# Optimization experiments

Measured on AMD Instinct MI355X. Metric: run time of the kernel, lower is better.

The kernel has to match this reference:

```python
import jax, jax.numpy as jnp
import numpy as np
import math

HEAD_DIM = 256
NUM_HEADS = 8
NUM_KV_HEADS = 1
ROPE_THETA = 10000.0


def _rope_cos_sin(position_ids, dim, base, dtype):
    # inv_freq: [dim//2]
    inv_freq = 1.0 / (base ** (jnp.arange(0, dim, 2, dtype=jnp.float32) / dim))
    # freqs: [B, S, dim//2]
    freqs = position_ids.astype(jnp.float32)[..., None] * inv_freq[None, None, :]
    emb = jnp.concatenate([freqs, freqs], axis=-1)  # [B, S, dim]
    return jnp.cos(emb).astype(dtype), jnp.sin(emb).astype(dtype)


def _rotate_half(x):
    half = x.shape[-1] // 2
    return jnp.concatenate([-x[..., half:], x[..., :half]], axis=-1)


def setup_inputs() -> dict:
    key = jax.random.key(0)
    ks = jax.random.split(key, 6)
    B, S, H = 2, 2048, 2048
    hidden_states = jax.random.normal(ks[0], (B, S, H), dtype=jnp.float32)
    attention_mask = jnp.zeros((B, 1, S, S), dtype=jnp.float32)
    position_ids = jnp.arange(B * S, dtype=jnp.int64).reshape(B, S) % S
    wq = jax.random.normal(ks[1], (H, NUM_HEADS * HEAD_DIM), dtype=jnp.float32) * 0.02
    wk = jax.random.normal(ks[2], (H, NUM_KV_HEADS * HEAD_DIM), dtype=jnp.float32) * 0.02
    wv = jax.random.normal(ks[3], (H, NUM_KV_HEADS * HEAD_DIM), dtype=jnp.float32) * 0.02
    wo = jax.random.normal(ks[4], (NUM_HEADS * HEAD_DIM, H), dtype=jnp.float32) * 0.02
    return {"hidden_states": hidden_states, "attention_mask": attention_mask,
            "position_ids": position_ids, "wq": wq, "wk": wk, "wv": wv, "wo": wo}


def reference(hidden_states, attention_mask, position_ids, wq, wk, wv, wo):
    B, S, _ = hidden_states.shape
    q = (hidden_states @ wq).reshape(B, S, NUM_HEADS, HEAD_DIM).transpose(0, 2, 1, 3)
    k = (hidden_states @ wk).reshape(B, S, NUM_KV_HEADS, HEAD_DIM).transpose(0, 2, 1, 3)
    v = (hidden_states @ wv).reshape(B, S, NUM_KV_HEADS, HEAD_DIM).transpose(0, 2, 1, 3)

    cos, sin = _rope_cos_sin(position_ids, HEAD_DIM, ROPE_THETA, hidden_states.dtype)
    cos = cos[:, None, :, :]  # [B,1,S,D]
    sin = sin[:, None, :, :]
    q = q * cos + _rotate_half(q) * sin
    k = k * cos + _rotate_half(k) * sin

    # repeat_kv (GQA/MQA expansion)
    n_rep = NUM_HEADS // NUM_KV_HEADS
    k = jnp.repeat(k, n_rep, axis=1)  # [B,H,S,D]
    v = jnp.repeat(v, n_rep, axis=1)

    scores = jnp.einsum('bhqd,bhkd->bhqk', q, k) / math.sqrt(HEAD_DIM)
    scores = scores + attention_mask
    probs = jax.nn.softmax(scores.astype(jnp.float32), axis=-1).astype(q.dtype)
    attn = jnp.einsum('bhqk,bhkd->bhqd', probs, v)  # [B,H,S,D]
    attn = attn.transpose(0, 2, 1, 3).reshape(B, S, NUM_HEADS * HEAD_DIM)
    return attn @ wo
```

## Files before the change

kernel.cpp:

```cpp
#include <hip/hip_runtime.h>
#include <hip/hip_bf16.h>

typedef unsigned short u16;
using f32x4  = __attribute__((ext_vector_type(4))) float;
using bf16x8 = __attribute__((ext_vector_type(8))) __bf16;
using u16x8  = __attribute__((ext_vector_type(8))) unsigned short;
using u16x4  = __attribute__((ext_vector_type(4))) unsigned short;

__device__ __forceinline__ float bf2f(u16 v) {
  union { unsigned u; float f; } x; x.u = ((unsigned)v) << 16; return x.f;
}
__device__ __forceinline__ u16 f2bf(float f) {
  union { float f; unsigned u; } x; x.f = f;
  unsigned r = x.u + 0x7fffu + ((x.u >> 16) & 1u);
  return (u16)(r >> 16);
}
__device__ __forceinline__ void async_load16(const u16* g, u16* l) {
  __builtin_amdgcn_global_load_lds(
      (const __attribute__((address_space(1))) unsigned int*)g,
      (__attribute__((address_space(3))) unsigned int*)l, 16, 0, 0);
}
__device__ __forceinline__ float fexp2(float x) {
#if __has_builtin(__builtin_amdgcn_exp2f)
  return __builtin_amdgcn_exp2f(x);
#else
  return exp2f(x);
#endif
}
__device__ __forceinline__ float vmax4(f32x4 v) {
  return fmaxf(fmaxf(v[0], v[1]), fmaxf(v[2], v[3]));
}
__device__ __forceinline__ int swz_col(int col, int rowk) {
  return (col & ~63) | ((((col >> 3) & 7) ^ rowk) << 3) | (col & 7);
}

__global__ __launch_bounds__(256) void cast_f32_bf16_sw(const float* __restrict__ in,
                                                        u16* __restrict__ out) {
  long i = ((long)blockIdx.x * 256 + threadIdx.x) * 8;
  int m = (int)(i >> 11);
  int col = (int)(i & 2047);
  float4 a = *(const float4*)(in + i);
  float4 b = *(const float4*)(in + i + 4);
  u16x8 v;
  v[0] = f2bf(a.x); v[1] = f2bf(a.y); v[2] = f2bf(a.z); v[3] = f2bf(a.w);
  v[4] = f2bf(b.x); v[5] = f2bf(b.y); v[6] = f2bf(b.z); v[7] = f2bf(b.w);
  *(u16x8*)(out + ((long)m << 11) + swz_col(col, m & 7)) = v;
}

__global__ __launch_bounds__(256) void trans_all(const float* __restrict__ wq,
                                                 const float* __restrict__ wk,
                                                 const float* __restrict__ wv,
                                                 const float* __restrict__ wo,
                                                 u16* __restrict__ wqkvT, u16* __restrict__ woT) {
  const int z = blockIdx.z, bx = blockIdx.x, by = blockIdx.y;
  if (z == 1 && bx >= 64) return;
  const float* src; int srs; u16* dst;
  const int R0 = bx * 32;
  if (z == 0) {
    if (R0 < 2048)      { src = wq + R0;          srs = 2048; }
    else if (R0 < 2304) { src = wk + (R0 - 2048); srs = 256;  }
    else                { src = wv + (R0 - 2304); srs = 256;  }
    dst = wqkvT;
  } else { src = wo + R0; srs = 2048; dst = woT; }
  __shared__ float t[32][33];
  int tx = threadIdx.x, ty = threadIdx.y;
  int br = by * 32;
#pragma unroll
  for (int i = 0; i < 32; i += 8)
    t[ty + i][tx] = src[(long)(br + ty + i) * srs + tx];
  __syncthreads();
#pragma unroll
  for (int i = 0; i < 32; i += 8) {
    int R = R0 + ty + i, C = br + tx;
    dst[(long)R * 2048 + swz_col(C, R & 7)] = f2bf(t[tx][ty + i]);
  }
}

template <typename CT>
__global__ __launch_bounds__(256) void gemm_bt(const u16* __restrict__ A, const u16* __restrict__ Bt,
                                               CT* __restrict__ C, int M, int N, int K) {
  __shared__ __attribute__((aligned(16))) u16 sA[128 * 64];
  __shared__ __attribute__((aligned(16))) u16 sB[128 * 64];
  const int n0 = blockIdx.x * 128, m0 = blockIdx.y * 128;
  const int tid = threadIdx.x;
  const int w = tid >> 6, lane = tid & 63;
  const int l15 = lane & 15, quad = lane >> 4;
  const int wm = (w >> 1) * 64, wn = (w & 1) * 64;
  const int lrow = lane >> 3, lcol = (lane & 7) * 8;
  const u16* Ag = A + (long)(m0 + lrow) * K + lcol;
  const u16* Bg = Bt + (long)(n0 + lrow) * K + lcol;
  const int g0 = ((quad ^ (l15 & 7)) << 3);
  f32x4 acc[4][4] = {};
  for (int k0 = 0; k0 < K; k0 += 64) {
#pragma unroll
    for (int i = 0; i < 4; ++i) {
      int rr = (w * 4 + i) * 8;
      async_load16(Ag + (long)rr * K + k0, &sA[rr * 64]);
      async_load16(Bg + (long)rr * K + k0, &sB[rr * 64]);
    }
    __syncthreads();
#pragma unroll
    for (int kk2 = 0; kk2 < 2; ++kk2) {
      const int go = kk2 ? (g0 ^ 32) : g0;
      bf16x8 af[4], bf[4];
#pragma unroll
      for (int t = 0; t < 4; ++t) {
        af[t] = *(const bf16x8*)&sA[(wm + t * 16 + l15) * 64 + go];
        bf[t] = *(const bf16x8*)&sB[(wn + t * 16 + l15) * 64 + go];
      }
#pragma unroll
      for (int mt = 0; mt < 4; ++mt)
#pragma unroll
        for (int nt = 0; nt < 4; ++nt)
          acc[mt][nt] = __builtin_amdgcn_mfma_f32_16x16x32_bf16(af[mt], bf[nt], acc[mt][nt], 0, 0, 0);
    }
    __syncthreads();
  }
#pragma unroll
  for (int mt = 0; mt < 4; ++mt)
#pragma unroll
    for (int nt = 0; nt < 4; ++nt)
#pragma unroll
      for (int r = 0; r < 4; ++r) {
        long idx = (long)(m0 + wm + mt * 16 + quad * 4 + r) * N + (n0 + wn + nt * 16 + l15);
        if constexpr (sizeof(CT) == 4) C[idx] = acc[mt][nt][r];
        else                           C[idx] = f2bf(acc[mt][nt][r]);
      }
}

__global__ __launch_bounds__(256) void rope_pack(u16* __restrict__ qkv, u16* __restrict__ kp) {
  const int row = blockIdx.x;
  const int tid = threadIdx.x;
  const int d = tid & 127;
  const int s = row & 2047;
  float ang = (float)s * fexp2(-(float)d * 0.10381025296523007f);
  float sn, cs;
  sincosf(ang, &sn, &cs);
  long base = (long)row * 2560;
#pragma unroll
  for (int j = 0; j < 4; ++j) {
    int h = (tid >> 7) + j * 2;
    long p = base + h * 256 + d;
    float x0 = bf2f(qkv[p]), x1 = bf2f(qkv[p + 128]);
    qkv[p]       = f2bf(x0 * cs - x1 * sn);
    qkv[p + 128] = f2bf(x1 * cs + x0 * sn);
  }
  if (tid < 128) {
    long p = base + 2048 + d;
    float x0 = bf2f(qkv[p]), x1 = bf2f(qkv[p + 128]);
    float y0 = x0 * cs - x1 * sn, y1 = x1 * cs + x0 * sn;
    int b = row >> 11, t = (row >> 6) & 31, r = row & 63;
    long sw = (r >> 1) & 7;
    long tb = (long)(b * 32 + t) * 8 * 2048;
#pragma unroll
    for (int u = 0; u < 2; ++u) {
      int D = d + u * 128;
      long off = tb + (long)(D >> 5) * 2048 + r * 32 + (D & 31);
      long off2 = (((off >> 3) ^ sw) << 3) | (off & 7);
      kp[off2] = f2bf(u ? y1 : y0);
    }
  }
}

__global__ __launch_bounds__(256) void pack_vt(const u16* __restrict__ qkv, u16* __restrict__ vp) {
  __shared__ u16 sm[32][40];
  int x = blockIdx.x, y = blockIdx.y, b = blockIdx.z;
  int tx = threadIdx.x, ty = threadIdx.y;
  long inrow = (long)b * 2048 + (y >> 1) * 64 + (y & 1) * 32;
#pragma unroll
  for (int i = 0; i < 32; i += 8)
    sm[ty + i][tx] = qkv[(inrow + ty + i) * 2560 + 2304 + x * 32 + tx];
  __syncthreads();
  long obase = ((long)(b * 32 + (y >> 1)) * 2 + (y & 1)) * 8192 + (long)x * 1024;
#pragma unroll
  for (int i = 0; i < 32; i += 8) {
    long el = obase + (ty + i) * 32 + tx;
    el ^= (long)((((ty + i) >> 1) & 7) << 3);
    vp[el] = sm[tx][ty + i];
  }
}

__global__ __launch_bounds__(512) void flash_attn(const u16* __restrict__ qkv,
                                                  const u16* __restrict__ kp,
                                                  const u16* __restrict__ vp,
                                                  u16* __restrict__ attn) {
  const int qt = blockIdx.x, h = blockIdx.y, b = blockIdx.z;
  const int tid = threadIdx.x, w = tid >> 6, lane = tid & 63;
  const int l15 = lane & 15, quad = lane >> 4;
  __shared__ __attribute__((aligned(16))) u16 sK[2][16384];
  __shared__ __attribute__((aligned(16))) u16 sV[2][16384];
  __shared__ __attribute__((aligned(16))) u16 sP[8][1152];
  const long rowb = (long)b * 2048;
  const int qrow0 = qt * 128 + w * 16;
  const int swz_rd = (l15 >> 1) * 64 + ((((l15 & 1) << 2) | quad) ^ (l15 >> 1)) * 8;

  bf16x8 aq[8];
  {
    const u16* qp = qkv + (rowb + qrow0 + l15) * 2560 + h * 256 + quad * 8;
#pragma unroll
    for (int kk = 0; kk < 8; ++kk) aq[kk] = *(const bf16x8*)(qp + kk * 32);
  }

  float m_i = -1e30f, l_i = 0.f;
  f32x4 accO[16] = {};
  const float SC = 0.09016844005556021f;

  u16* Pw = &sP[w][0];
  const u16* kpb = kp + (long)b * 32 * 16384;
  const u16* vpb = vp + (long)b * 32 * 16384;

#pragma unroll
  for (int j = 0; j < 4; ++j) {
    int base = (w * 4 + j) * 512;
    async_load16(kpb + base + lane * 8, &sK[0][base]);
    async_load16(vpb + base + lane * 8, &sV[0][base]);
  }
  __syncthreads();

  for (int it = 0; it < 32; ++it) {
    const int cur = it & 1;
    const int nx = (it < 31) ? it + 1 : 31;
    const u16* ktn = kpb + (long)nx * 16384;
    const u16* vtn = vpb + (long)nx * 16384;
#pragma unroll
    for (int j = 0; j < 4; ++j) {
      int base = (w * 4 + j) * 512;
      async_load16(ktn + base + lane * 8, &sK[cur ^ 1][base]);
      async_load16(vtn + base + lane * 8, &sV[cur ^ 1][base]);
    }
    f32x4 sc[4] = {};
#pragma unroll
    for (int kk = 0; kk < 8; ++kk)
#pragma unroll
      for (int nt = 0; nt < 2; ++nt) {
        bf16x8 bk = *(const bf16x8*)&sK[cur][kk * 2048 + nt * 512 + swz_rd];
        sc[nt] = __builtin_amdgcn_mfma_f32_16x16x32_bf16(bk, aq[kk], sc[nt], 0, 0, 0);
      }
#pragma unroll
    for (int kk = 0; kk < 8; ++kk)
#pragma unroll
      for (int nt = 2; nt < 4; ++nt) {
        bf16x8 bk = *(const bf16x8*)&sK[cur][kk * 2048 + nt * 512 + swz_rd];
        sc[nt] = __builtin_amdgcn_mfma_f32_16x16x32_bf16(bk, aq[kk], sc[nt], 0, 0, 0);
      }

    {
      float mx = fmaxf(vmax4(sc[0]), vmax4(sc[1])) * SC;
      float s1 = __shfl_xor(mx, 16, 64);
      float s2 = __shfl_xor(mx, 32, 64);
      float s3 = __shfl_xor(mx, 48, 64);
      mx = fmaxf(fmaxf(mx, s1), fmaxf(s2, s3));
      if (!__all(mx - m_i <= 8.f)) {
        float mnew = fmaxf(m_i, mx);
        float al = fexp2(m_i - mnew);
        m_i = mnew;
        l_i *= al;
#pragma unroll
        for (int r = 0; r < 4; ++r) {
          float ar = __shfl(al, quad * 4 + r, 16);
#pragma unroll
          for (int t = 0; t < 16; ++t) accO[t][r] *= ar;
        }
      }
      float rs = 0.f;
#pragma unroll
      for (int nt = 0; nt < 2; ++nt) {
        u16x4 pk;
#pragma unroll
        for (int r = 0; r < 4; ++r) {
          float pv = fexp2(sc[nt][r] * SC - m_i);
          rs += pv;
          pk[r] = f2bf(pv);
        }
        *(u16x4*)&Pw[l15 * 72 + nt * 16 + quad * 4] = pk;
      }
      l_i += rs;
    }
    asm volatile("s_waitcnt lgkmcnt(0)" ::: "memory");
    bf16x8 pa0 = *(const bf16x8*)&Pw[l15 * 72 + quad * 8];
#pragma unroll
    for (int t = 0; t < 16; ++t) {
      bf16x8 bv0 = *(const bf16x8*)&sV[cur][t * 512 + swz_rd];
      accO[t] = __builtin_amdgcn_mfma_f32_16x16x32_bf16(pa0, bv0, accO[t], 0, 0, 0);
    }
    {
      float mx = fmaxf(vmax4(sc[2]), vmax4(sc[3])) * SC;
      float s1 = __shfl_xor(mx, 16, 64);
      float s2 = __shfl_xor(mx, 32, 64);
      float s3 = __shfl_xor(mx, 48, 64);
      mx = fmaxf(fmaxf(mx, s1), fmaxf(s2, s3));
      if (!__all(mx - m_i <= 8.f)) {
        float mnew = fmaxf(m_i, mx);
        float al = fexp2(m_i - mnew);
        m_i = mnew;
        l_i *= al;
#pragma unroll
        for (int r = 0; r < 4; ++r) {
          float ar = __shfl(al, quad * 4 + r, 16);
#pragma unroll
          for (int t = 0; t < 16; ++t) accO[t][r] *= ar;
        }
      }
      float rs = 0.f;
#pragma unroll
      for (int nt = 2; nt < 4; ++nt) {
        u16x4 pk;
#pragma unroll
        for (int r = 0; r < 4; ++r) {
          float pv = fexp2(sc[nt][r] * SC - m_i);
          rs += pv;
          pk[r] = f2bf(pv);
        }
        *(u16x4*)&Pw[l15 * 72 + nt * 16 + quad * 4] = pk;
      }
      l_i += rs;
    }
    asm volatile("s_waitcnt lgkmcnt(0)" ::: "memory");
    bf16x8 pa1 = *(const bf16x8*)&Pw[l15 * 72 + 32 + quad * 8];
#pragma unroll
    for (int t = 0; t < 16; ++t) {
      bf16x8 bv1 = *(const bf16x8*)&sV[cur][8192 + t * 512 + swz_rd];
      accO[t] = __builtin_amdgcn_mfma_f32_16x16x32_bf16(pa1, bv1, accO[t], 0, 0, 0);
    }
    __syncthreads();
  }
  {
    float t1 = __shfl_xor(l_i, 16, 64);
    float t2 = __shfl_xor(l_i, 32, 64);
    float t3 = __shfl_xor(l_i, 48, 64);
    l_i = (l_i + t1) + (t2 + t3);
  }
#pragma unroll
  for (int r = 0; r < 4; ++r) {
    float lr = __shfl(l_i, quad * 4 + r, 16);
    float rinv = 1.f / lr;
    int key = (quad * 4 + r) & 7;
#pragma unroll
    for (int t = 0; t < 16; ++t) {
      int col = h * 256 + t * 16 + l15;
      attn[(rowb + qrow0 + quad * 4 + r) * 2048 + swz_col(col, key)] =
          f2bf(accO[t][r] * rinv);
    }
  }
}

extern "C" void kernel_launch(void* const* d_in, const int* in_sizes, int n_in,
                              void* d_out, int out_size, void* d_ws, size_t ws_size,
                              hipStream_t stream) {
  const float* hidden = (const float*)d_in[0];
  const float* wq = (const float*)d_in[3];
  const float* wk = (const float*)d_in[4];
  const float* wv = (const float*)d_in[5];
  const float* wo = (const float*)d_in[6];
  float* out = (float*)d_out;

  char* ws = (char*)d_ws;
  u16* QKV   = (u16*)(ws);
  u16* WqkvT = (u16*)(ws + 20971520);
  u16* Kp    = (u16*)(ws + 20971520);
  u16* Vp    = (u16*)(ws + 23068672);
  u16* WoT   = (u16*)(ws + 31457280);
  u16* HB    = (u16*)(ws + 39845888);
  u16* ATT   = (u16*)(ws + 39845888);

  cast_f32_bf16_sw<<<4096, 256, 0, stream>>>(hidden, HB);
  trans_all<<<dim3(80, 64, 2), dim3(32, 8), 0, stream>>>(wq, wk, wv, wo, WqkvT, WoT);

  gemm_bt<u16><<<dim3(20, 32), dim3(256), 0, stream>>>(HB, WqkvT, QKV, 4096, 2560, 2048);

  rope_pack<<<4096, 256, 0, stream>>>(QKV, Kp);
  pack_vt<<<dim3(8, 64, 2), dim3(32, 8), 0, stream>>>(QKV, Vp);

  flash_attn<<<dim3(16, 8, 2), dim3(512), 0, stream>>>(QKV, Kp, Vp, ATT);

  gemm_bt<float><<<dim3(16, 32), dim3(256), 0, stream>>>(ATT, WoT, out, 4096, 2048, 2048);
}
```

Measured before the change: 338.8 us.

## Process two 16-row query tiles per wave to reuse K/V LDS fragments

The flash attention kernel now runs 4 waves of 256 threads per block, and each wave handles 32 query rows as two independent 16-row sub-tiles with separate softmax state. Each K and V fragment read from shared memory feeds two MFMAs instead of one, halving LDS read traffic per FLOP. Each wave computes scores over the full 64-key tile before the softmax instead of two 32-key halves. The cost is roughly double the accumulator and Q register footprint (launch_bounds 256,1), fewer waves per CU to hide latency, and each thread issuing twice as many async K/V loads.

```diff
diff --git a/kernel.cpp b/kernel.cpp
--- a/kernel.cpp
+++ b/kernel.cpp
@@ -180,38 +180,43 @@
   }
 }
 
-__global__ __launch_bounds__(512) void flash_attn(const u16* __restrict__ qkv,
-                                                  const u16* __restrict__ kp,
-                                                  const u16* __restrict__ vp,
-                                                  u16* __restrict__ attn) {
+__global__ __launch_bounds__(256, 1) void flash_attn(const u16* __restrict__ qkv,
+                                                     const u16* __restrict__ kp,
+                                                     const u16* __restrict__ vp,
+                                                     u16* __restrict__ attn) {
   const int qt = blockIdx.x, h = blockIdx.y, b = blockIdx.z;
   const int tid = threadIdx.x, w = tid >> 6, lane = tid & 63;
   const int l15 = lane & 15, quad = lane >> 4;
   __shared__ __attribute__((aligned(16))) u16 sK[2][16384];
   __shared__ __attribute__((aligned(16))) u16 sV[2][16384];
-  __shared__ __attribute__((aligned(16))) u16 sP[8][1152];
+  __shared__ __attribute__((aligned(16))) u16 sP[4][2304];
   const long rowb = (long)b * 2048;
-  const int qrow0 = qt * 128 + w * 16;
+  const int qrow0 = qt * 128 + w * 32;
   const int swz_rd = (l15 >> 1) * 64 + ((((l15 & 1) << 2) | quad) ^ (l15 >> 1)) * 8;
 
-  bf16x8 aq[8];
+  bf16x8 aqA[8], aqB[8];
   {
-    const u16* qp = qkv + (rowb + qrow0 + l15) * 2560 + h * 256 + quad * 8;
-#pragma unroll
-    for (int kk = 0; kk < 8; ++kk) aq[kk] = *(const bf16x8*)(qp + kk * 32);
-  }
-
-  float m_i = -1e30f, l_i = 0.f;
-  f32x4 accO[16] = {};
+    const u16* qpA = qkv + (rowb + qrow0 + l15) * 2560 + h * 256 + quad * 8;
+    const u16* qpB = qpA + 16 * 2560;
+#pragma unroll
+    for (int kk = 0; kk < 8; ++kk) {
+      aqA[kk] = *(const bf16x8*)(qpA + kk * 32);
+      aqB[kk] = *(const bf16x8*)(qpB + kk * 32);
+    }
+  }
+
+  float mA = -1e30f, lA = 0.f, mB = -1e30f, lB = 0.f;
+  f32x4 accA[16] = {}, accB[16] = {};
   const float SC = 0.09016844005556021f;
 
-  u16* Pw = &sP[w][0];
+  u16* PwA = &sP[w][0];
+  u16* PwB = &sP[w][1152];
   const u16* kpb = kp + (long)b * 32 * 16384;
   const u16* vpb = vp + (long)b * 32 * 16384;
 
 #pragma unroll
-  for (int j = 0; j < 4; ++j) {
-    int base = (w * 4 + j) * 512;
+  for (int j = 0; j < 8; ++j) {
+    int base = (w * 8 + j) * 512;
     async_load16(kpb + base + lane * 8, &sK[0][base]);
     async_load16(vpb + base + lane * 8, &sV[0][base]);
   }
@@ -223,123 +228,131 @@
     const u16* ktn = kpb + (long)nx * 16384;
     const u16* vtn = vpb + (long)nx * 16384;
 #pragma unroll
-    for (int j = 0; j < 4; ++j) {
-      int base = (w * 4 + j) * 512;
+    for (int j = 0; j < 8; ++j) {
+      int base = (w * 8 + j) * 512;
       async_load16(ktn + base + lane * 8, &sK[cur ^ 1][base]);
       async_load16(vtn + base + lane * 8, &sV[cur ^ 1][base]);
     }
-    f32x4 sc[4] = {};
+    f32x4 scA[4] = {}, scB[4] = {};
 #pragma unroll
     for (int kk = 0; kk < 8; ++kk)
 #pragma unroll
-      for (int nt = 0; nt < 2; ++nt) {
+      for (int nt = 0; nt < 4; ++nt) {
         bf16x8 bk = *(const bf16x8*)&sK[cur][kk * 2048 + nt * 512 + swz_rd];
-        sc[nt] = __builtin_amdgcn_mfma_f32_16x16x32_bf16(bk, aq[kk], sc[nt], 0, 0, 0);
-      }
-#pragma unroll
-    for (int kk = 0; kk < 8; ++kk)
-#pragma unroll
-      for (int nt = 2; nt < 4; ++nt) {
-        bf16x8 bk = *(const bf16x8*)&sK[cur][kk * 2048 + nt * 512 + swz_rd];
-        sc[nt] = __builtin_amdgcn_mfma_f32_16x16x32_bf16(bk, aq[kk], sc[nt], 0, 0, 0);
+        scA[nt] = __builtin_amdgcn_mfma_f32_16x16x32_bf16(bk, aqA[kk], scA[nt], 0, 0, 0);
+        scB[nt] = __builtin_amdgcn_mfma_f32_16x16x32_bf16(bk, aqB[kk], scB[nt], 0, 0, 0);
       }
 
     {
-      float mx = fmaxf(vmax4(sc[0]), vmax4(sc[1])) * SC;
+      float mx = fmaxf(fmaxf(vmax4(scA[0]), vmax4(scA[1])),
+                       fmaxf(vmax4(scA[2]), vmax4(scA[3]))) * SC;
       float s1 = __shfl_xor(mx, 16, 64);
       float s2 = __shfl_xor(mx, 32, 64);
       float s3 = __shfl_xor(mx, 48, 64);
       mx = fmaxf(fmaxf(mx, s1), fmaxf(s2, s3));
-      if (!__all(mx - m_i <= 8.f)) {
-        float mnew = fmaxf(m_i, mx);
-        float al = fexp2(m_i - mnew);
-        m_i = mnew;
-        l_i *= al;
+      if (!__all(mx - mA <= 8.f)) {
+        float mnew = fmaxf(mA, mx);
+        float al = fexp2(mA - mnew);
+        mA = mnew;
+        lA *= al;
 #pragma unroll
         for (int r = 0; r < 4; ++r) {
           float ar = __shfl(al, quad * 4 + r, 16);
 #pragma unroll
-          for (int t = 0; t < 16; ++t) accO[t][r] *= ar;
+          for (int t = 0; t < 16; ++t) accA[t][r] *= ar;
         }
       }
       float rs = 0.f;
 #pragma unroll
-      for (int nt = 0; nt < 2; ++nt) {
+      for (int nt = 0; nt < 4; ++nt) {
         u16x4 pk;
 #pragma unroll
         for (int r = 0; r < 4; ++r) {
-          float pv = fexp2(sc[nt][r] * SC - m_i);
+          float pv = fexp2(scA[nt][r] * SC - mA);
           rs += pv;
           pk[r] = f2bf(pv);
         }
-        *(u16x4*)&Pw[l15 * 72 + nt * 16 + quad * 4] = pk;
-      }
-      l_i += rs;
+        *(u16x4*)&PwA[l15 * 72 + nt * 16 + quad * 4] = pk;
+      }
+      lA += rs;
     }
     asm volatile("s_waitcnt lgkmcnt(0)" ::: "memory");
-    bf16x8 pa0 = *(const bf16x8*)&Pw[l15 * 72 + quad * 8];
+    bf16x8 paA0 = *(const bf16x8*)&PwA[l15 * 72 + quad * 8];
+    bf16x8 paA1 = *(const bf16x8*)&PwA[l15 * 72 + 32 + quad * 8];
+    bf16x8 bv0[16];
 #pragma unroll
     for (int t = 0; t < 16; ++t) {
-      bf16x8 bv0 = *(const bf16x8*)&sV[cur][t * 512 + swz_rd];
-      accO[t] = __builtin_amdgcn_mfma_f32_16x16x32_bf16(pa0, bv0, accO[t], 0, 0, 0);
+      bv0[t] = *(const bf16x8*)&sV[cur][t * 512 + swz_rd];
+      accA[t] = __builtin_amdgcn_mfma_f32_16x16x32_bf16(paA0, bv0[t], accA[t], 0, 0, 0);
     }
     {
-      float mx = fmaxf(vmax4(sc[2]), vmax4(sc[3])) * SC;
+      float mx = fmaxf(fmaxf(vmax4(scB[0]), vmax4(scB[1])),
+                       fmaxf(vmax4(scB[2]), vmax4(scB[3]))) * SC;
       float s1 = __shfl_xor(mx, 16, 64);
       float s2 = __shfl_xor(mx, 32, 64);
       float s3 = __shfl_xor(mx, 48, 64);
       mx = fmaxf(fmaxf(mx, s1), fmaxf(s2, s3));
-      if (!__all(mx - m_i <= 8.f)) {
-        float mnew = fmaxf(m_i, mx);
-        float al = fexp2(m_i - mnew);
-        m_i = mnew;
-        l_i *= al;
+      if (!__all(mx - mB <= 8.f)) {
+        float mnew = fmaxf(mB, mx);
+        float al = fexp2(mB - mnew);
+        mB = mnew;
+        lB *= al;
 #pragma unroll
         for (int r = 0; r < 4; ++r) {
           float ar = __shfl(al, quad * 4 + r, 16);
 #pragma unroll
-          for (int t = 0; t < 16; ++t) accO[t][r] *= ar;
+          for (int t = 0; t < 16; ++t) accB[t][r] *= ar;
         }
       }
       float rs = 0.f;
 #pragma unroll
-      for (int nt = 2; nt < 4; ++nt) {
+      for (int nt = 0; nt < 4; ++nt) {
         u16x4 pk;
 #pragma unroll
         for (int r = 0; r < 4; ++r) {
-          float pv = fexp2(sc[nt][r] * SC - m_i);
+          float pv = fexp2(scB[nt][r] * SC - mB);
           rs += pv;
           pk[r] = f2bf(pv);
         }
-        *(u16x4*)&Pw[l15 * 72 + nt * 16 + quad * 4] = pk;
-      }
-      l_i += rs;
+        *(u16x4*)&PwB[l15 * 72 + nt * 16 + quad * 4] = pk;
+      }
+      lB += rs;
     }
     asm volatile("s_waitcnt lgkmcnt(0)" ::: "memory");
-    bf16x8 pa1 = *(const bf16x8*)&Pw[l15 * 72 + 32 + quad * 8];
+    bf16x8 paB0 = *(const bf16x8*)&PwB[l15 * 72 + quad * 8];
+    bf16x8 paB1 = *(const bf16x8*)&PwB[l15 * 72 + 32 + quad * 8];
 #pragma unroll
     for (int t = 0; t < 16; ++t) {
+      accB[t] = __builtin_amdgcn_mfma_f32_16x16x32_bf16(paB0, bv0[t], accB[t], 0, 0, 0);
       bf16x8 bv1 = *(const bf16x8*)&sV[cur][8192 + t * 512 + swz_rd];
-      accO[t] = __builtin_amdgcn_mfma_f32_16x16x32_bf16(pa1, bv1, accO[t], 0, 0, 0);
+      accA[t] = __builtin_amdgcn_mfma_f32_16x16x32_bf16(paA1, bv1, accA[t], 0, 0, 0);
+      accB[t] = __builtin_amdgcn_mfma_f32_16x16x32_bf16(paB1, bv1, accB[t], 0, 0, 0);
     }
     __syncthreads();
   }
   {
-    float t1 = __shfl_xor(l_i, 16, 64);
-    float t2 = __shfl_xor(l_i, 32, 64);
-    float t3 = __shfl_xor(l_i, 48, 64);
-    l_i = (l_i + t1) + (t2 + t3);
+    float t1 = __shfl_xor(lA, 16, 64);
+    float t2 = __shfl_xor(lA, 32, 64);
+    float t3 = __shfl_xor(lA, 48, 64);
+    lA = (lA + t1) + (t2 + t3);
+    t1 = __shfl_xor(lB, 16, 64);
+    t2 = __shfl_xor(lB, 32, 64);
+    t3 = __shfl_xor(lB, 48, 64);
+    lB = (lB + t1) + (t2 + t3);
   }
 #pragma unroll
   for (int r = 0; r < 4; ++r) {
-    float lr = __shfl(l_i, quad * 4 + r, 16);
-    float rinv = 1.f / lr;
+    float lrA = __shfl(lA, quad * 4 + r, 16);
+    float lrB = __shfl(lB, quad * 4 + r, 16);
+    float rinvA = 1.f / lrA;
+    float rinvB = 1.f / lrB;
     int key = (quad * 4 + r) & 7;
 #pragma unroll
     for (int t = 0; t < 16; ++t) {
       int col = h * 256 + t * 16 + l15;
-      attn[(rowb + qrow0 + quad * 4 + r) * 2048 + swz_col(col, key)] =
-          f2bf(accO[t][r] * rinv);
+      int sc_ = swz_col(col, key);
+      attn[(rowb + qrow0 + quad * 4 + r) * 2048 + sc_]      = f2bf(accA[t][r] * rinvA);
+      attn[(rowb + qrow0 + 16 + quad * 4 + r) * 2048 + sc_] = f2bf(accB[t][r] * rinvB);
     }
   }
 }
@@ -371,7 +384,7 @@
   rope_pack<<<4096, 256, 0, stream>>>(QKV, Kp);
   pack_vt<<<dim3(8, 64, 2), dim3(32, 8), 0, stream>>>(QKV, Vp);
 
-  flash_attn<<<dim3(16, 8, 2), dim3(512), 0, stream>>>(QKV, Kp, Vp, ATT);
+  flash_attn<<<dim3(16, 8, 2), dim3(256), 0, stream>>>(QKV, Kp, Vp, ATT);
 
   gemm_bt<float><<<dim3(16, 32), dim3(256), 0, stream>>>(ATT, WoT, out, 4096, 2048, 2048);
 }
```

New measurement: 370.4 us. +9.3%, slower.

## Replace GEMM with 256x256-tile double-buffered ping-pong pipelined kernel

Applied to the files above, without the earlier changes.

Both projection GEMMs move to a new kernel with 256x256 output tiles, 512 threads and double-buffered LDS. The loads for the next K-step are issued in four slices between MFMA phases, with explicit barriers, waitcnts and setprio so copy and compute overlap. The aim is to hide global-to-LDS latency and raise the compute per LDS byte. The larger tiles shrink the grids to 160 and 128 blocks, fewer than the CU count. The roughly 128KB of LDS per block also limits occupancy, so some CUs may sit idle.

```diff
diff --git a/kernel.cpp b/kernel.cpp
--- a/kernel.cpp
+++ b/kernel.cpp
@@ -77,47 +77,109 @@
 }
 
 template <typename CT>
-__global__ __launch_bounds__(256) void gemm_bt(const u16* __restrict__ A, const u16* __restrict__ Bt,
-                                               CT* __restrict__ C, int M, int N, int K) {
-  __shared__ __attribute__((aligned(16))) u16 sA[128 * 64];
-  __shared__ __attribute__((aligned(16))) u16 sB[128 * 64];
-  const int n0 = blockIdx.x * 128, m0 = blockIdx.y * 128;
+__global__ __launch_bounds__(512, 2) void gemm_bt256(const u16* __restrict__ A,
+                                                     const u16* __restrict__ Bt,
+                                                     CT* __restrict__ C, int M, int N, int K) {
+  __shared__ __attribute__((aligned(16))) u16 sA[2][256 * 64];
+  __shared__ __attribute__((aligned(16))) u16 sB[2][256 * 64];
+  const int n0 = blockIdx.x * 256, m0 = blockIdx.y * 256;
   const int tid = threadIdx.x;
   const int w = tid >> 6, lane = tid & 63;
   const int l15 = lane & 15, quad = lane >> 4;
-  const int wm = (w >> 1) * 64, wn = (w & 1) * 64;
+  const int wm = (w >> 2) * 128, wn = (w & 3) * 64;
   const int lrow = lane >> 3, lcol = (lane & 7) * 8;
-  const u16* Ag = A + (long)(m0 + lrow) * K + lcol;
-  const u16* Bg = Bt + (long)(n0 + lrow) * K + lcol;
+  const u16* Ag = A + (long)(m0 + w * 32 + lrow) * K + lcol;
+  const u16* Bg = Bt + (long)(n0 + w * 32 + lrow) * K + lcol;
   const int g0 = ((quad ^ (l15 & 7)) << 3);
-  f32x4 acc[4][4] = {};
-  for (int k0 = 0; k0 < K; k0 += 64) {
-#pragma unroll
-    for (int i = 0; i < 4; ++i) {
-      int rr = (w * 4 + i) * 8;
-      async_load16(Ag + (long)rr * K + k0, &sA[rr * 64]);
-      async_load16(Bg + (long)rr * K + k0, &sB[rr * 64]);
-    }
-    __syncthreads();
-#pragma unroll
-    for (int kk2 = 0; kk2 < 2; ++kk2) {
-      const int go = kk2 ? (g0 ^ 32) : g0;
-      bf16x8 af[4], bf[4];
-#pragma unroll
-      for (int t = 0; t < 4; ++t) {
-        af[t] = *(const bf16x8*)&sA[(wm + t * 16 + l15) * 64 + go];
-        bf[t] = *(const bf16x8*)&sB[(wn + t * 16 + l15) * 64 + go];
-      }
-#pragma unroll
-      for (int mt = 0; mt < 4; ++mt)
-#pragma unroll
-        for (int nt = 0; nt < 4; ++nt)
-          acc[mt][nt] = __builtin_amdgcn_mfma_f32_16x16x32_bf16(af[mt], bf[nt], acc[mt][nt], 0, 0, 0);
-    }
-    __syncthreads();
-  }
-#pragma unroll
-  for (int mt = 0; mt < 4; ++mt)
+  const int g1 = g0 ^ 32;
+  f32x4 acc[8][4] = {};
+
+  const auto stage = [&](int t, int bf, int i) {
+    const int k0 = t * 64;
+    async_load16(Ag + (long)(i * 8) * K + k0, &sA[bf][(w * 32 + i * 8) * 64]);
+    async_load16(Bg + (long)(i * 8) * K + k0, &sB[bf][(w * 32 + i * 8) * 64]);
+  };
+
+#pragma unroll
+  for (int i = 0; i < 4; ++i) stage(0, 0, i);
+  asm volatile("s_waitcnt vmcnt(0)" ::: "memory");
+  __syncthreads();
+
+  const int T = K >> 6;
+  for (int t = 0; t < T; ++t) {
+    const int cur = t & 1;
+    const bool pf = (t + 1 < T);
+    bf16x8 af[4], bfr[4];
+#pragma unroll
+    for (int mt = 0; mt < 4; ++mt)
+      af[mt] = *(const bf16x8*)&sA[cur][(wm + mt * 16 + l15) * 64 + g0];
+#pragma unroll
+    for (int nt = 0; nt < 4; ++nt)
+      bfr[nt] = *(const bf16x8*)&sB[cur][(wn + nt * 16 + l15) * 64 + g0];
+    if (pf) stage(t + 1, cur ^ 1, 0);
+    __builtin_amdgcn_s_barrier();
+    asm volatile("s_waitcnt lgkmcnt(0)" ::: "memory");
+    __builtin_amdgcn_sched_barrier(0);
+    __builtin_amdgcn_s_setprio(1);
+#pragma unroll
+    for (int mt = 0; mt < 4; ++mt)
+#pragma unroll
+      for (int nt = 0; nt < 4; ++nt)
+        acc[mt][nt] = __builtin_amdgcn_mfma_f32_16x16x32_bf16(af[mt], bfr[nt], acc[mt][nt], 0, 0, 0);
+    __builtin_amdgcn_s_setprio(0);
+    __builtin_amdgcn_s_barrier();
+#pragma unroll
+    for (int mt = 0; mt < 4; ++mt)
+      af[mt] = *(const bf16x8*)&sA[cur][(wm + 64 + mt * 16 + l15) * 64 + g0];
+    if (pf) stage(t + 1, cur ^ 1, 1);
+    __builtin_amdgcn_s_barrier();
+    asm volatile("s_waitcnt lgkmcnt(0)" ::: "memory");
+    __builtin_amdgcn_sched_barrier(0);
+    __builtin_amdgcn_s_setprio(1);
+#pragma unroll
+    for (int mt = 0; mt < 4; ++mt)
+#pragma unroll
+      for (int nt = 0; nt < 4; ++nt)
+        acc[mt + 4][nt] = __builtin_amdgcn_mfma_f32_16x16x32_bf16(af[mt], bfr[nt], acc[mt + 4][nt], 0, 0, 0);
+    __builtin_amdgcn_s_setprio(0);
+    __builtin_amdgcn_s_barrier();
+#pragma unroll
+    for (int mt = 0; mt < 4; ++mt)
+      af[mt] = *(const bf16x8*)&sA[cur][(wm + mt * 16 + l15) * 64 + g1];
+#pragma unroll
+    for (int nt = 0; nt < 4; ++nt)
+      bfr[nt] = *(const bf16x8*)&sB[cur][(wn + nt * 16 + l15) * 64 + g1];
+    if (pf) stage(t + 1, cur ^ 1, 2);
+    __builtin_amdgcn_s_barrier();
+    asm volatile("s_waitcnt lgkmcnt(0)" ::: "memory");
+    __builtin_amdgcn_sched_barrier(0);
+    __builtin_amdgcn_s_setprio(1);
+#pragma unroll
+    for (int mt = 0; mt < 4; ++mt)
+#pragma unroll
+      for (int nt = 0; nt < 4; ++nt)
+        acc[mt][nt] = __builtin_amdgcn_mfma_f32_16x16x32_bf16(af[mt], bfr[nt], acc[mt][nt], 0, 0, 0);
+    __builtin_amdgcn_s_setprio(0);
+    __builtin_amdgcn_s_barrier();
+#pragma unroll
+    for (int mt = 0; mt < 4; ++mt)
+      af[mt] = *(const bf16x8*)&sA[cur][(wm + 64 + mt * 16 + l15) * 64 + g1];
+    if (pf) stage(t + 1, cur ^ 1, 3);
+    __builtin_amdgcn_s_barrier();
+    asm volatile("s_waitcnt lgkmcnt(0)" ::: "memory");
+    __builtin_amdgcn_sched_barrier(0);
+    __builtin_amdgcn_s_setprio(1);
+#pragma unroll
+    for (int mt = 0; mt < 4; ++mt)
+#pragma unroll
+      for (int nt = 0; nt < 4; ++nt)
+        acc[mt + 4][nt] = __builtin_amdgcn_mfma_f32_16x16x32_bf16(af[mt], bfr[nt], acc[mt + 4][nt], 0, 0, 0);
+    __builtin_amdgcn_s_setprio(0);
+    asm volatile("s_waitcnt vmcnt(0)" ::: "memory");
+    __builtin_amdgcn_s_barrier();
+  }
+#pragma unroll
+  for (int mt = 0; mt < 8; ++mt)
 #pragma unroll
     for (int nt = 0; nt < 4; ++nt)
 #pragma unroll
@@ -366,12 +428,12 @@
   cast_f32_bf16_sw<<<4096, 256, 0, stream>>>(hidden, HB);
   trans_all<<<dim3(80, 64, 2), dim3(32, 8), 0, stream>>>(wq, wk, wv, wo, WqkvT, WoT);
 
-  gemm_bt<u16><<<dim3(20, 32), dim3(256), 0, stream>>>(HB, WqkvT, QKV, 4096, 2560, 2048);
+  gemm_bt256<u16><<<dim3(10, 16), dim3(512), 0, stream>>>(HB, WqkvT, QKV, 4096, 2560, 2048);
 
   rope_pack<<<4096, 256, 0, stream>>>(QKV, Kp);
   pack_vt<<<dim3(8, 64, 2), dim3(32, 8), 0, stream>>>(QKV, Vp);
 
   flash_attn<<<dim3(16, 8, 2), dim3(512), 0, stream>>>(QKV, Kp, Vp, ATT);
 
-  gemm_bt<float><<<dim3(16, 32), dim3(256), 0, stream>>>(ATT, WoT, out, 4096, 2048, 2048);
-}
+  gemm_bt256<float><<<dim3(8, 16), dim3(512), 0, stream>>>(ATT, WoT, out, 4096, 2048, 2048);
+}
```

Measured after the change: 363.6 us. 7.3% more time.

## Double-buffer GEMM LDS loads with wider 512-thread tiles and MFMA priority

Applied to the files above, without the earlier changes.

Replaces the single-buffered 128x128 GEMM with a templated kernel that uses 8 waves and a 128 x (NTW*64) tile. Global-to-LDS loads for the next K step are issued into a second buffer while the current one is consumed. s_setprio is raised around the MFMA block. The aim is to hide load latency, drop one barrier per iteration, and cut grid size (8x32 blocks for both projections). In exchange LDS use grows to double buffers of up to 288x64 bf16, which may limit occupancy, and the grids now cover fewer CUs.

```diff
diff --git a/kernel.cpp b/kernel.cpp
--- a/kernel.cpp
+++ b/kernel.cpp
@@ -76,50 +76,68 @@
   }
 }
 
-template <typename CT>
-__global__ __launch_bounds__(256) void gemm_bt(const u16* __restrict__ A, const u16* __restrict__ Bt,
-                                               CT* __restrict__ C, int M, int N, int K) {
-  __shared__ __attribute__((aligned(16))) u16 sA[128 * 64];
-  __shared__ __attribute__((aligned(16))) u16 sB[128 * 64];
-  const int n0 = blockIdx.x * 128, m0 = blockIdx.y * 128;
+template <int NTW, typename CT>
+__global__ __launch_bounds__(512, 2) void gemm_v4(const u16* __restrict__ A,
+                                                  const u16* __restrict__ Bt,
+                                                  CT* __restrict__ C, int M, int N, int K) {
+  constexpr int BN  = NTW * 64;
+  constexpr int RT  = 128 + BN;
+  constexpr int CPW = RT / 64;
+  __shared__ __attribute__((aligned(16))) u16 sBuf[2][RT * 64];
+  const int n0 = blockIdx.x * BN, m0 = blockIdx.y * 128;
   const int tid = threadIdx.x;
   const int w = tid >> 6, lane = tid & 63;
   const int l15 = lane & 15, quad = lane >> 4;
-  const int wm = (w >> 1) * 64, wn = (w & 1) * 64;
+  const int wm = (w >> 2) * 64, wn = (w & 3) * (NTW * 16);
   const int lrow = lane >> 3, lcol = (lane & 7) * 8;
   const u16* Ag = A + (long)(m0 + lrow) * K + lcol;
   const u16* Bg = Bt + (long)(n0 + lrow) * K + lcol;
   const int g0 = ((quad ^ (l15 & 7)) << 3);
-  f32x4 acc[4][4] = {};
-  for (int k0 = 0; k0 < K; k0 += 64) {
-#pragma unroll
-    for (int i = 0; i < 4; ++i) {
-      int rr = (w * 4 + i) * 8;
-      async_load16(Ag + (long)rr * K + k0, &sA[rr * 64]);
-      async_load16(Bg + (long)rr * K + k0, &sB[rr * 64]);
+  f32x4 acc[4][NTW] = {};
+
+  const auto stage = [&](int t, int bf) {
+    const int k0 = t * 64;
+#pragma unroll
+    for (int j = 0; j < CPW; ++j) {
+      const int chunk = w * CPW + j;
+      const u16* src = (chunk < 16)
+          ? (Ag + (long)(chunk * 8) * K + k0)
+          : (Bg + (long)((chunk - 16) * 8) * K + k0);
+      async_load16(src, &sBuf[bf][chunk * 512]);
+    }
+  };
+
+  stage(0, 0);
+  __syncthreads();
+
+  const int T = K >> 6;
+  for (int t = 0; t < T; ++t) {
+    const int cur = t & 1;
+    if (t + 1 < T) stage(t + 1, cur ^ 1);
+#pragma unroll
+    for (int kk = 0; kk < 2; ++kk) {
+      const int g = kk ? (g0 ^ 32) : g0;
+      bf16x8 af[4], bfr[NTW];
+#pragma unroll
+      for (int mt = 0; mt < 4; ++mt)
+        af[mt] = *(const bf16x8*)&sBuf[cur][(wm + mt * 16 + l15) * 64 + g];
+#pragma unroll
+      for (int nt = 0; nt < NTW; ++nt)
+        bfr[nt] = *(const bf16x8*)&sBuf[cur][(128 + wn + nt * 16 + l15) * 64 + g];
+      __builtin_amdgcn_s_setprio(1);
+#pragma unroll
+      for (int mt = 0; mt < 4; ++mt)
+#pragma unroll
+        for (int nt = 0; nt < NTW; ++nt)
+          acc[mt][nt] = __builtin_amdgcn_mfma_f32_16x16x32_bf16(af[mt], bfr[nt], acc[mt][nt], 0, 0, 0);
+      __builtin_amdgcn_s_setprio(0);
     }
     __syncthreads();
-#pragma unroll
-    for (int kk2 = 0; kk2 < 2; ++kk2) {
-      const int go = kk2 ? (g0 ^ 32) : g0;
-      bf16x8 af[4], bf[4];
-#pragma unroll
-      for (int t = 0; t < 4; ++t) {
-        af[t] = *(const bf16x8*)&sA[(wm + t * 16 + l15) * 64 + go];
-        bf[t] = *(const bf16x8*)&sB[(wn + t * 16 + l15) * 64 + go];
-      }
-#pragma unroll
-      for (int mt = 0; mt < 4; ++mt)
-#pragma unroll
-        for (int nt = 0; nt < 4; ++nt)
-          acc[mt][nt] = __builtin_amdgcn_mfma_f32_16x16x32_bf16(af[mt], bf[nt], acc[mt][nt], 0, 0, 0);
-    }
-    __syncthreads();
   }
 #pragma unroll
   for (int mt = 0; mt < 4; ++mt)
 #pragma unroll
-    for (int nt = 0; nt < 4; ++nt)
+    for (int nt = 0; nt < NTW; ++nt)
 #pragma unroll
       for (int r = 0; r < 4; ++r) {
         long idx = (long)(m0 + wm + mt * 16 + quad * 4 + r) * N + (n0 + wn + nt * 16 + l15);
@@ -366,12 +384,12 @@
   cast_f32_bf16_sw<<<4096, 256, 0, stream>>>(hidden, HB);
   trans_all<<<dim3(80, 64, 2), dim3(32, 8), 0, stream>>>(wq, wk, wv, wo, WqkvT, WoT);
 
-  gemm_bt<u16><<<dim3(20, 32), dim3(256), 0, stream>>>(HB, WqkvT, QKV, 4096, 2560, 2048);
+  gemm_v4<5, u16><<<dim3(8, 32), dim3(512), 0, stream>>>(HB, WqkvT, QKV, 4096, 2560, 2048);
 
   rope_pack<<<4096, 256, 0, stream>>>(QKV, Kp);
   pack_vt<<<dim3(8, 64, 2), dim3(32, 8), 0, stream>>>(QKV, Vp);
 
   flash_attn<<<dim3(16, 8, 2), dim3(512), 0, stream>>>(QKV, Kp, Vp, ATT);
 
-  gemm_bt<float><<<dim3(16, 32), dim3(256), 0, stream>>>(ATT, WoT, out, 4096, 2048, 2048);
-}
+  gemm_v4<4, float><<<dim3(8, 32), dim3(512), 0, stream>>>(ATT, WoT, out, 4096, 2048, 2048);
+}
```

Result: no change. 338.8 us (-0.0%).
